# Kernel optimization log

Measured on AMD Instinct MI355X. Metric: run time of the kernel, lower is better.

The kernel has to match this reference:

```python
import jax, jax.numpy as jnp
import numpy as np


def setup_inputs() -> dict:
    key = jax.random.key(0)
    ks = jax.random.split(key, 6)
    N, C, T, V = 32, 64, 128, 25
    F = C * T * V  # 204800
    H = 256
    E = 4
    stdv0 = 1.0 / np.sqrt(F)
    stdv1 = 1.0 / np.sqrt(H)
    stdvA = 1.0 / np.sqrt(V)
    return {
        "x": jax.random.normal(ks[0], (N, C, T, V), dtype=jnp.float32),
        "W0": jax.random.uniform(ks[1], (F, H), jnp.float32, -stdv0, stdv0),
        "b0": jnp.zeros((H,), jnp.float32),
        "W1": jax.random.uniform(ks[2], (H, H), jnp.float32, -stdv1, stdv1),
        "b1": jnp.zeros((H,), jnp.float32),
        "W2": jax.random.uniform(ks[3], (H, E), jnp.float32, -stdv1, stdv1),
        "b2": jnp.zeros((E,), jnp.float32),
        "A": jax.random.uniform(ks[4], (E, T, V, V), jnp.float32, -stdvA, stdvA),
    }


def reference(x, W0, b0, W1, b1, W2, b2, A):
    N = x.shape[0]
    # Gating MLP (dropout treated as identity / eval mode)
    g = x.reshape(N, -1)                      # [N, C*T*V]
    h = jax.nn.elu(g @ W0 + b0)               # [N, 256]
    h = jax.nn.elu(h @ W1 + b1)               # [N, 256]
    logits = h @ W2 + b2                      # [N, 4]
    w = jax.nn.softmax(logits, axis=1)        # [N, 4]
    # Mixture of adjacency experts: AS[n,t,v,w] = sum_e w[n,e] * A[e,t,v,w]
    AS = jnp.einsum('ne,etvw->ntvw', w, A)    # [N, T, V, V]
    # Batched graph convolution
    out = jnp.einsum('nctv,ntvw->nctw', x, AS)
    return out
```

## Files before the change

### kernel.cpp

```cpp
#include <hip/hip_runtime.h>
#include <math.h>

#define Nn 32
#define Cc 64
#define Tt 128
#define Vv 25
#define Kk 204800
#define Hh 256
#define Ee 4
#define KC 256
#define KB 16
#define NSTEP (KC / KB)
#define NBLK_A 800

__device__ __forceinline__ float elu1(float v) { return v > 0.0f ? v : expm1f(v); }

typedef const __attribute__((address_space(1))) void* gvp;
typedef __attribute__((address_space(3))) void* lvp;
__device__ __forceinline__ void gl_lds16(const void* g, void* l) {
  __builtin_amdgcn_global_load_lds((gvp)g, (lvp)l, 16, 0, 0);
}

__global__ __launch_bounds__(256) void kA(const float* __restrict__ x,
                                          const float* __restrict__ W0,
                                          float* __restrict__ partials) {
  __shared__ float xs[Nn][KC];
  __shared__ float wbuf[2][KB][Hh];
  const int tid  = threadIdx.x;
  const int lane = tid & 63;
  const int wv   = tid >> 6;
  const int b  = blockIdx.x;
  const int k0 = b * KC;

  for (int r = wv; r < Nn; r += 4)
    gl_lds16(x + (size_t)r * Kk + k0 + lane * 4, &xs[r][0]);
  for (int r = wv; r < KB; r += 4)
    gl_lds16(W0 + (size_t)(k0 + r) * Hh + lane * 4, &wbuf[0][r][0]);
  __syncthreads();

  const int hg = tid & 31;
  const int np = tid >> 5;
  const int h0 = hg * 8;
  const int n0 = np * 4;

  float acc[4][8];
  #pragma unroll
  for (int i = 0; i < 4; ++i)
    #pragma unroll
    for (int c = 0; c < 8; ++c) acc[i][c] = 0.0f;

  for (int step = 0; step < NSTEP; ++step) {
    const int cur = step & 1;
    if (step + 1 < NSTEP) {
      const int kb = (step + 1) * KB;
      for (int r = wv; r < KB; r += 4)
        gl_lds16(W0 + (size_t)(k0 + kb + r) * Hh + lane * 4, &wbuf[cur ^ 1][r][0]);
    }
    const int kbase = step * KB;
    #pragma unroll
    for (int kk = 0; kk < KB; kk += 4) {
      float4 xv[4];
      #pragma unroll
      for (int i = 0; i < 4; ++i)
        xv[i] = *(const float4*)&xs[n0 + i][kbase + kk];
      #pragma unroll
      for (int u = 0; u < 4; ++u) {
        const float* wp = &wbuf[cur][kk + u][h0];
        float4 wa = *(const float4*)(wp);
        float4 wb = *(const float4*)(wp + 4);
        #pragma unroll
        for (int i = 0; i < 4; ++i) {
          float xu = (u == 0) ? xv[i].x : (u == 1) ? xv[i].y : (u == 2) ? xv[i].z : xv[i].w;
          acc[i][0] = fmaf(xu, wa.x, acc[i][0]);
          acc[i][1] = fmaf(xu, wa.y, acc[i][1]);
          acc[i][2] = fmaf(xu, wa.z, acc[i][2]);
          acc[i][3] = fmaf(xu, wa.w, acc[i][3]);
          acc[i][4] = fmaf(xu, wb.x, acc[i][4]);
          acc[i][5] = fmaf(xu, wb.y, acc[i][5]);
          acc[i][6] = fmaf(xu, wb.z, acc[i][6]);
          acc[i][7] = fmaf(xu, wb.w, acc[i][7]);
        }
      }
    }
    __syncthreads();
  }

  #pragma unroll
  for (int i = 0; i < 4; ++i) {
    float* pp = partials + ((size_t)(b * Nn + n0 + i) << 8) + h0;
    *(float4*)(pp)     = make_float4(acc[i][0], acc[i][1], acc[i][2], acc[i][3]);
    *(float4*)(pp + 4) = make_float4(acc[i][4], acc[i][5], acc[i][6], acc[i][7]);
  }
}

__global__ __launch_bounds__(256) void kB1(const float* __restrict__ partials,
                                           const float* __restrict__ b0,
                                           float* __restrict__ hb) {
  const int n  = blockIdx.x >> 3;
  const int hc = blockIdx.x & 7;
  const int tid = threadIdx.x;
  const int hl = tid & 31;
  const int bsub = tid >> 5;
  const int h = hc * 32 + hl;
  float s = 0.0f;
  for (int j = 0; j < 100; ++j) {
    int b = bsub * 100 + j;
    s += partials[((size_t)(b * Nn + n) << 8) + h];
  }
  __shared__ float red[8][32];
  red[bsub][hl] = s;
  __syncthreads();
  if (tid < 32) {
    float tot = 0.0f;
    #pragma unroll
    for (int sI = 0; sI < 8; ++sI) tot += red[sI][tid];
    int hh = hc * 32 + tid;
    hb[n * Hh + hh] = elu1(tot + b0[hh]);
  }
}

__global__ __launch_bounds__(256) void kB2(const float* __restrict__ hb,
                                           const float* __restrict__ W1,
                                           const float* __restrict__ b1,
                                           const float* __restrict__ W2,
                                           const float* __restrict__ b2,
                                           float* __restrict__ wgt) {
  const int n = blockIdx.x;
  const int tid = threadIdx.x;
  __shared__ float hbs[Hh];
  hbs[tid] = hb[n * Hh + tid];
  __syncthreads();
  float s = b1[tid];
  for (int j = 0; j < Hh; ++j) s = fmaf(hbs[j], W1[j * Hh + tid], s);
  float h2 = elu1(s);
  float le[Ee];
  #pragma unroll
  for (int e = 0; e < Ee; ++e) le[e] = h2 * W2[tid * Ee + e];
  __shared__ float red[Ee][4];
  const int lane = tid & 63;
  const int wid  = tid >> 6;
  #pragma unroll
  for (int e = 0; e < Ee; ++e) {
    float v = le[e];
    for (int off = 32; off > 0; off >>= 1) v += __shfl_down(v, off, 64);
    if (lane == 0) red[e][wid] = v;
  }
  __syncthreads();
  if (tid == 0) {
    float lg[Ee];
    float m = -1e30f;
    #pragma unroll
    for (int e = 0; e < Ee; ++e) {
      lg[e] = red[e][0] + red[e][1] + red[e][2] + red[e][3] + b2[e];
      m = fmaxf(m, lg[e]);
    }
    float den = 0.0f;
    #pragma unroll
    for (int e = 0; e < Ee; ++e) { lg[e] = expf(lg[e] - m); den += lg[e]; }
    float inv = 1.0f / den;
    #pragma unroll
    for (int e = 0; e < Ee; ++e) wgt[n * Ee + e] = lg[e] * inv;
  }
}

#define ASW 28
#define XTS 68
__global__ __launch_bounds__(256) void kC(const float* __restrict__ x,
                                          const float* __restrict__ A,
                                          const float* __restrict__ wgt,
                                          float* __restrict__ out) {
  const int blk = blockIdx.x;
  const int n  = blk >> 6;
  const int tp = blk & 63;
  const int tid = threadIdx.x;
  const int tsub = tid >> 7;
  const int tl = tid & 127;
  const int t = tp * 2 + tsub;

  __shared__ float AS[2][Vv][ASW];
  __shared__ float xT[2][Vv][XTS];

  float wv[Ee];
  #pragma unroll
  for (int e = 0; e < Ee; ++e) wv[e] = wgt[n * Ee + e];

  for (int idx = tl; idx < Vv * ASW; idx += 128) {
    int v = idx / ASW;
    int w = idx - v * ASW;
    float s = 0.0f;
    if (w < Vv) {
      #pragma unroll
      for (int e = 0; e < Ee; ++e)
        s = fmaf(wv[e], A[((size_t)(e * Tt + t) * Vv + v) * Vv + w], s);
    }
    AS[tsub][v][w] = s;
  }
  const float* xb = x + (size_t)n * (Cc * Tt * Vv) + (size_t)t * Vv;
  for (int idx = tl; idx < Cc * Vv; idx += 128) {
    int c = idx / Vv;
    int v = idx - c * Vv;
    xT[tsub][v][c] = xb[(size_t)c * (Tt * Vv) + v];
  }
  __syncthreads();

  const int ct = tl & 15;
  const int wq = tl >> 4;
  if (wq < 7) {
    const int c0 = ct * 4;
    const int w0 = wq * 4;
    float acc[4][4];
    #pragma unroll
    for (int i = 0; i < 4; ++i)
      #pragma unroll
      for (int j = 0; j < 4; ++j) acc[i][j] = 0.0f;
    #pragma unroll 5
    for (int v = 0; v < Vv; ++v) {
      float4 a4 = *(const float4*)&AS[tsub][v][w0];
      float4 x4 = *(const float4*)&xT[tsub][v][c0];
      const float xr[4] = {x4.x, x4.y, x4.z, x4.w};
      const float ar[4] = {a4.x, a4.y, a4.z, a4.w};
      #pragma unroll
      for (int i = 0; i < 4; ++i)
        #pragma unroll
        for (int j = 0; j < 4; ++j)
          acc[i][j] = fmaf(xr[i], ar[j], acc[i][j]);
    }
    #pragma unroll
    for (int i = 0; i < 4; ++i) {
      int c = c0 + i;
      float* ob = out + ((size_t)(n * Cc + c) * Tt + t) * Vv;
      #pragma unroll
      for (int j = 0; j < 4; ++j) {
        int w = w0 + j;
        if (w < Vv) ob[w] = acc[i][j];
      }
    }
  }
}

extern "C" void kernel_launch(void* const* d_in, const int* in_sizes, int n_in,
                              void* d_out, int out_size, void* d_ws, size_t ws_size,
                              hipStream_t stream) {
  const float* x  = (const float*)d_in[0];
  const float* W0 = (const float*)d_in[1];
  const float* b0 = (const float*)d_in[2];
  const float* W1 = (const float*)d_in[3];
  const float* b1 = (const float*)d_in[4];
  const float* W2 = (const float*)d_in[5];
  const float* b2 = (const float*)d_in[6];
  const float* A  = (const float*)d_in[7];
  float* out = (float*)d_out;

  float* partials = (float*)d_ws;
  float* hb  = partials + (size_t)NBLK_A * Nn * Hh;
  float* wgt = hb + Nn * Hh;

  kA <<<NBLK_A,  256, 0, stream>>>(x, W0, partials);
  kB1<<<256,     256, 0, stream>>>(partials, b0, hb);
  kB2<<<Nn,      256, 0, stream>>>(hb, W1, b1, W2, b2, wgt);
  kC <<<Nn * 64, 256, 0, stream>>>(x, A, wgt, out);
}
```

Baseline: 379.1 us.

## Stream W0 directly into registers with double-buffered prefetch in kA

The GEMV-like kA kernel no longer stages W0 tiles through LDS with per-step block barriers. Each thread now loads its own 8-column slice of W0 straight from global memory into registers, double-buffered across two 4-row groups, and only x stays in LDS. This removes the LDS write/read traffic for W0 and the repeated __syncthreads, and launch_bounds now asks for 3 blocks per CU. In exchange, eight threads load the same W0 elements and depend on cache to merge them, and the added prefetch registers may raise register pressure.

```diff
diff --git a/kernel.cpp b/kernel.cpp
--- a/kernel.cpp
+++ b/kernel.cpp
@@ -9,8 +9,6 @@
 #define Hh 256
 #define Ee 4
 #define KC 256
-#define KB 16
-#define NSTEP (KC / KB)
 #define NBLK_A 800
 
 __device__ __forceinline__ float elu1(float v) { return v > 0.0f ? v : expm1f(v); }
@@ -21,11 +19,12 @@
   __builtin_amdgcn_global_load_lds((gvp)g, (lvp)l, 16, 0, 0);
 }
 
-__global__ __launch_bounds__(256) void kA(const float* __restrict__ x,
-                                          const float* __restrict__ W0,
-                                          float* __restrict__ partials) {
+struct WGrp { float4 a[4]; float4 b[4]; };
+
+__global__ __launch_bounds__(256, 3) void kA(const float* __restrict__ x,
+                                             const float* __restrict__ W0,
+                                             float* __restrict__ partials) {
   __shared__ float xs[Nn][KC];
-  __shared__ float wbuf[2][KB][Hh];
   const int tid  = threadIdx.x;
   const int lane = tid & 63;
   const int wv   = tid >> 6;
@@ -34,14 +33,12 @@
 
   for (int r = wv; r < Nn; r += 4)
     gl_lds16(x + (size_t)r * Kk + k0 + lane * 4, &xs[r][0]);
-  for (int r = wv; r < KB; r += 4)
-    gl_lds16(W0 + (size_t)(k0 + r) * Hh + lane * 4, &wbuf[0][r][0]);
-  __syncthreads();
 
   const int hg = tid & 31;
   const int np = tid >> 5;
   const int h0 = hg * 8;
   const int n0 = np * 4;
+  const float* W0p = W0 + (size_t)k0 * Hh + h0;
 
   float acc[4][8];
   #pragma unroll
@@ -49,25 +46,31 @@
     #pragma unroll
     for (int c = 0; c < 8; ++c) acc[i][c] = 0.0f;
 
-  for (int step = 0; step < NSTEP; ++step) {
-    const int cur = step & 1;
-    if (step + 1 < NSTEP) {
-      const int kb = (step + 1) * KB;
-      for (int r = wv; r < KB; r += 4)
-        gl_lds16(W0 + (size_t)(k0 + kb + r) * Hh + lane * 4, &wbuf[cur ^ 1][r][0]);
-    }
-    const int kbase = step * KB;
-    #pragma unroll
-    for (int kk = 0; kk < KB; kk += 4) {
+  WGrp g0, g1;
+  #pragma unroll
+  for (int u = 0; u < 4; ++u) {
+    const float* wp = W0p + (size_t)u * Hh;
+    g0.a[u] = *(const float4*)(wp);
+    g0.b[u] = *(const float4*)(wp + 4);
+  }
+  __syncthreads();
+
+  #pragma unroll 1
+  for (int kk = 0; kk < KC; kk += 8) {
+    #pragma unroll
+    for (int u = 0; u < 4; ++u) {
+      const float* wp = W0p + (size_t)(kk + 4 + u) * Hh;
+      g1.a[u] = *(const float4*)(wp);
+      g1.b[u] = *(const float4*)(wp + 4);
+    }
+    {
       float4 xv[4];
       #pragma unroll
       for (int i = 0; i < 4; ++i)
-        xv[i] = *(const float4*)&xs[n0 + i][kbase + kk];
+        xv[i] = *(const float4*)&xs[n0 + i][kk];
       #pragma unroll
       for (int u = 0; u < 4; ++u) {
-        const float* wp = &wbuf[cur][kk + u][h0];
-        float4 wa = *(const float4*)(wp);
-        float4 wb = *(const float4*)(wp + 4);
+        float4 wa = g0.a[u], wb = g0.b[u];
         #pragma unroll
         for (int i = 0; i < 4; ++i) {
           float xu = (u == 0) ? xv[i].x : (u == 1) ? xv[i].y : (u == 2) ? xv[i].z : xv[i].w;
@@ -82,7 +85,37 @@
         }
       }
     }
-    __syncthreads();
+    {
+      const int nk = (kk + 8 < KC) ? (kk + 8) : 0;
+      #pragma unroll
+      for (int u = 0; u < 4; ++u) {
+        const float* wp = W0p + (size_t)(nk + u) * Hh;
+        g0.a[u] = *(const float4*)(wp);
+        g0.b[u] = *(const float4*)(wp + 4);
+      }
+    }
+    {
+      float4 xv[4];
+      #pragma unroll
+      for (int i = 0; i < 4; ++i)
+        xv[i] = *(const float4*)&xs[n0 + i][kk + 4];
+      #pragma unroll
+      for (int u = 0; u < 4; ++u) {
+        float4 wa = g1.a[u], wb = g1.b[u];
+        #pragma unroll
+        for (int i = 0; i < 4; ++i) {
+          float xu = (u == 0) ? xv[i].x : (u == 1) ? xv[i].y : (u == 2) ? xv[i].z : xv[i].w;
+          acc[i][0] = fmaf(xu, wa.x, acc[i][0]);
+          acc[i][1] = fmaf(xu, wa.y, acc[i][1]);
+          acc[i][2] = fmaf(xu, wa.z, acc[i][2]);
+          acc[i][3] = fmaf(xu, wa.w, acc[i][3]);
+          acc[i][4] = fmaf(xu, wb.x, acc[i][4]);
+          acc[i][5] = fmaf(xu, wb.y, acc[i][5]);
+          acc[i][6] = fmaf(xu, wb.z, acc[i][6]);
+          acc[i][7] = fmaf(xu, wb.w, acc[i][7]);
+        }
+      }
+    }
   }
 
   #pragma unroll
```

New measurement: 416.7 us. 9.9% more time.
